# Performance work log

Hardware: AMD Instinct MI355X
Metric: run time of the kernel (lower is better)

The kernel has to match this reference:

```python
import jax, jax.numpy as jnp
import numpy as np

DIM0, DIMO, WIDTH, DEPTH = 64, 16, 128, 6  # depth = number of weight matrices
N = 524288


def setup_inputs() -> dict:
    key = jax.random.key(0)
    ks = jax.random.split(key, DEPTH + 1)
    x = jax.random.normal(ks[0], (N, DIM0), dtype=jnp.float32)
    bd0 = 1.0 / np.sqrt(DIM0)   # first layer init bound (per torch code)
    bd = 1.0 / np.sqrt(WIDTH)   # remaining layers init bound
    W0 = jax.random.uniform(ks[1], (DIM0, WIDTH), minval=-bd0, maxval=bd0, dtype=jnp.float32)
    W1 = jax.random.uniform(ks[2], (WIDTH, WIDTH), minval=-bd, maxval=bd, dtype=jnp.float32)
    W2 = jax.random.uniform(ks[3], (WIDTH, WIDTH), minval=-bd, maxval=bd, dtype=jnp.float32)
    W3 = jax.random.uniform(ks[4], (WIDTH, WIDTH), minval=-bd, maxval=bd, dtype=jnp.float32)
    W4 = jax.random.uniform(ks[5], (WIDTH, WIDTH), minval=-bd, maxval=bd, dtype=jnp.float32)
    W5 = jax.random.uniform(ks[6], (WIDTH, DIMO), minval=-bd, maxval=bd, dtype=jnp.float32)
    bias = jnp.zeros((DIMO,), dtype=jnp.float32)
    return {"x": x, "W0": W0, "W1": W1, "W2": W2, "W3": W3, "W4": W4, "W5": W5, "bias": bias}


def reference(x, W0, W1, W2, W3, W4, W5, bias):
    # Fully-fused MLP math: matmul (no bias) + ReLU for every layer except the
    # last (output_activation='None'); then cast back to x dtype and add bias.
    h = jax.nn.relu(x @ W0)
    h = jax.nn.relu(h @ W1)
    h = jax.nn.relu(h @ W2)
    h = jax.nn.relu(h @ W3)
    h = jax.nn.relu(h @ W4)
    out = (h @ W5).astype(x.dtype) + bias
    return out
```

## Files before the change

### kernel.cpp

```cpp
#include <hip/hip_runtime.h>
#include <stdint.h>


typedef __bf16 bf16x8 __attribute__((ext_vector_type(8)));
typedef __bf16 bf16x4 __attribute__((ext_vector_type(4)));
typedef float  floatx4 __attribute__((ext_vector_type(4)));

constexpr int NS   = 524288;
constexpr int TILE = 128;
constexpr int NBLK = NS / TILE;

constexpr int WTOT = 9472;

__global__ void prep_weights(const float* __restrict__ W0, const float* __restrict__ W1,
                             const float* __restrict__ W2, const float* __restrict__ W3,
                             const float* __restrict__ W4, const float* __restrict__ W5,
                             bf16x8* __restrict__ ws) {
  int gid = blockIdx.x * blockDim.x + threadIdx.x;
  if (gid >= WTOT) return;
  const float* Wsrc; int nout, KT, base;
  if (gid < 1024)      { Wsrc = W0; nout = 128; KT = 2; base = 0;    }
  else if (gid < 3072) { Wsrc = W1; nout = 128; KT = 4; base = 1024; }
  else if (gid < 5120) { Wsrc = W2; nout = 128; KT = 4; base = 3072; }
  else if (gid < 7168) { Wsrc = W3; nout = 128; KT = 4; base = 5120; }
  else if (gid < 9216) { Wsrc = W4; nout = 128; KT = 4; base = 7168; }
  else                 { Wsrc = W5; nout = 16;  KT = 4; base = 9216; }
  int id  = gid - base;
  int p   = id & 63;
  int l15 = p & 15;
  int g   = p >> 4;
  int blk = id >> 6;
  int kt  = blk % KT;
  int it  = blk / KT;
  int row = it * 16 + l15;
  int kc  = kt * 4 + g;
  bf16x8 v;
#pragma unroll
  for (int j = 0; j < 8; ++j)
    v[j] = (__bf16)Wsrc[(8 * kc + j) * nout + row];
  ws[gid] = v;
}

__device__ __forceinline__ void zero_acc(floatx4 acc[4][4]) {
  floatx4 z = {0.f, 0.f, 0.f, 0.f};
#pragma unroll
  for (int i = 0; i < 4; ++i)
#pragma unroll
    for (int j = 0; j < 4; ++j) acc[i][j] = z;
}

template <int KT>
__device__ __forceinline__ void layer_mm(const bf16x8* __restrict__ wg,
                                         const bf16x8* Hb, floatx4 acc[4][4],
                                         int n_base, int l15, int g, int lane) {
#pragma unroll
  for (int kt = 0; kt < KT; ++kt) {
    const int cx = (kt * 4 + g) ^ (l15 & 7);
    bf16x8 a[4], b[4];
#pragma unroll
    for (int i = 0; i < 4; ++i) a[i] = wg[((i * KT + kt) << 6) + lane];
#pragma unroll
    for (int i = 0; i < 4; ++i) b[i] = Hb[(n_base + 16 * i + l15) * 16 + cx];
#pragma unroll
    for (int ot = 0; ot < 4; ++ot)
#pragma unroll
      for (int nt = 0; nt < 4; ++nt)
        acc[ot][nt] = __builtin_amdgcn_mfma_f32_16x16x32_bf16(a[ot], b[nt], acc[ot][nt], 0, 0, 0);
  }
}

__device__ __forceinline__ void write_h(bf16x4* H8, const floatx4 acc[4][4],
                                        int m_base, int n_base, int l15, int g) {
#pragma unroll
  for (int ot = 0; ot < 4; ++ot) {
    int ob    = m_base + 16 * ot + 4 * g;
    int phys8 = (((ob >> 3) ^ (l15 & 7)) << 1) | ((ob >> 2) & 1);
#pragma unroll
    for (int nt = 0; nt < 4; ++nt) {
      int s = n_base + 16 * nt + l15;
      floatx4 v = acc[ot][nt];
      bf16x4 h;
      h[0] = (__bf16)fmaxf(v[0], 0.0f);
      h[1] = (__bf16)fmaxf(v[1], 0.0f);
      h[2] = (__bf16)fmaxf(v[2], 0.0f);
      h[3] = (__bf16)fmaxf(v[3], 0.0f);
      H8[s * 32 + phys8] = h;
    }
  }
}

__global__ void __launch_bounds__(256, 4) mlp_kernel(const float* __restrict__ x,
                                                     const float* __restrict__ bias,
                                                     const bf16x8* __restrict__ wimg,
                                                     float* __restrict__ out) {
  __shared__ bf16x8 Hbuf[TILE * 16];

  const int t    = threadIdx.x;
  const int lane = t & 63;
  const int w    = t >> 6;
  const int l15  = lane & 15;
  const int g    = lane >> 4;
  const int m_half = w & 1;
  const int m_base = m_half * 64;
  const int n_base = (w >> 1) * 64;
  const int tile = blockIdx.x;

  const float* xt = x + (size_t)tile * TILE * 64;
#pragma unroll
  for (int i = 0; i < 4; ++i) {
    int f2 = t + 256 * i;
    int s = f2 >> 3, c = f2 & 7;
    const floatx4* src = (const floatx4*)(xt + f2 * 8);
    floatx4 lo = src[0], hi = src[1];
    bf16x8 v;
    v[0] = (__bf16)lo[0]; v[1] = (__bf16)lo[1]; v[2] = (__bf16)lo[2]; v[3] = (__bf16)lo[3];
    v[4] = (__bf16)hi[0]; v[5] = (__bf16)hi[1]; v[6] = (__bf16)hi[2]; v[7] = (__bf16)hi[3];
    Hbuf[s * 16 + (c ^ (s & 7))] = v;
  }
  __syncthreads();

  floatx4 acc[4][4];

  zero_acc(acc);
  layer_mm<2>(wimg + m_half * 512, Hbuf, acc, n_base, l15, g, lane);
  __syncthreads();
  write_h((bf16x4*)Hbuf, acc, m_base, n_base, l15, g);
  __syncthreads();

  constexpr int WOFF[5] = {1024, 3072, 5120, 7168, 9216};
#pragma unroll
  for (int l = 0; l < 4; ++l) {
    zero_acc(acc);
    layer_mm<4>(wimg + WOFF[l] + m_half * 1024, Hbuf, acc, n_base, l15, g, lane);
    __syncthreads();
    write_h((bf16x4*)Hbuf, acc, m_base, n_base, l15, g);
    __syncthreads();
  }

  floatx4 a5[2];
  {
    floatx4 z = {0.f, 0.f, 0.f, 0.f};
    a5[0] = z; a5[1] = z;
  }
  const int n5 = w * 32;
#pragma unroll
  for (int kt = 0; kt < 4; ++kt) {
    int cx = (kt * 4 + g) ^ (l15 & 7);
    bf16x8 a = wimg[9216 + (kt << 6) + lane];
#pragma unroll
    for (int nt = 0; nt < 2; ++nt) {
      bf16x8 b = Hbuf[(n5 + 16 * nt + l15) * 16 + cx];
      a5[nt] = __builtin_amdgcn_mfma_f32_16x16x32_bf16(a, b, a5[nt], 0, 0, 0);
    }
  }
  floatx4 bv = *(const floatx4*)(bias + 4 * g);
  floatx4* outv = (floatx4*)out;
#pragma unroll
  for (int nt = 0; nt < 2; ++nt) {
    int s = tile * TILE + n5 + 16 * nt + l15;
    outv[s * 4 + g] = a5[nt] + bv;
  }
}

extern "C" void kernel_launch(void* const* d_in, const int* in_sizes, int n_in,
                              void* d_out, int out_size, void* d_ws, size_t ws_size,
                              hipStream_t stream) {
  (void)in_sizes; (void)n_in; (void)out_size; (void)ws_size;
  const float* x    = (const float*)d_in[0];
  const float* W0   = (const float*)d_in[1];
  const float* W1   = (const float*)d_in[2];
  const float* W2   = (const float*)d_in[3];
  const float* W3   = (const float*)d_in[4];
  const float* W4   = (const float*)d_in[5];
  const float* W5   = (const float*)d_in[6];
  const float* bias = (const float*)d_in[7];
  bf16x8* ws = (bf16x8*)d_ws;

  prep_weights<<<(WTOT + 255) / 256, 256, 0, stream>>>(W0, W1, W2, W3, W4, W5, ws);
  mlp_kernel<<<NBLK, 256, 0, stream>>>(x, bias, (const bf16x8*)ws, (float*)d_out);
}
```

Baseline: 282.7 us.

## Give each wave full output width over its own rows and drop block barriers

Repartitions the per-layer GEMM so each wave computes all 128 output features for its own 32 samples, so hidden activations in shared memory are private per wave. This lets all __syncthreads between layers be removed, and the input staging is likewise done per wave. In exchange each wave loads twice as many weight fragments per k-step, and the occupancy hint is lowered from 4 to 3.

```diff
diff --git a/kernel.cpp b/kernel.cpp
--- a/kernel.cpp
+++ b/kernel.cpp
@@ -41,42 +41,42 @@
   ws[gid] = v;
 }
 
-__device__ __forceinline__ void zero_acc(floatx4 acc[4][4]) {
+__device__ __forceinline__ void zero_acc(floatx4 acc[8][2]) {
   floatx4 z = {0.f, 0.f, 0.f, 0.f};
 #pragma unroll
-  for (int i = 0; i < 4; ++i)
-#pragma unroll
-    for (int j = 0; j < 4; ++j) acc[i][j] = z;
+  for (int i = 0; i < 8; ++i) {
+    acc[i][0] = z; acc[i][1] = z;
+  }
 }
 
 template <int KT>
 __device__ __forceinline__ void layer_mm(const bf16x8* __restrict__ wg,
-                                         const bf16x8* Hb, floatx4 acc[4][4],
+                                         const bf16x8* Hb, floatx4 acc[8][2],
                                          int n_base, int l15, int g, int lane) {
 #pragma unroll
   for (int kt = 0; kt < KT; ++kt) {
     const int cx = (kt * 4 + g) ^ (l15 & 7);
-    bf16x8 a[4], b[4];
+    bf16x8 a[8], b[2];
 #pragma unroll
-    for (int i = 0; i < 4; ++i) a[i] = wg[((i * KT + kt) << 6) + lane];
+    for (int i = 0; i < 8; ++i) a[i] = wg[((i * KT + kt) << 6) + lane];
+    b[0] = Hb[(n_base + l15) * 16 + cx];
+    b[1] = Hb[(n_base + 16 + l15) * 16 + cx];
 #pragma unroll
-    for (int i = 0; i < 4; ++i) b[i] = Hb[(n_base + 16 * i + l15) * 16 + cx];
+    for (int ot = 0; ot < 8; ++ot)
 #pragma unroll
-    for (int ot = 0; ot < 4; ++ot)
-#pragma unroll
-      for (int nt = 0; nt < 4; ++nt)
+      for (int nt = 0; nt < 2; ++nt)
         acc[ot][nt] = __builtin_amdgcn_mfma_f32_16x16x32_bf16(a[ot], b[nt], acc[ot][nt], 0, 0, 0);
   }
 }
 
-__device__ __forceinline__ void write_h(bf16x4* H8, const floatx4 acc[4][4],
-                                        int m_base, int n_base, int l15, int g) {
+__device__ __forceinline__ void write_h(bf16x4* H8, const floatx4 acc[8][2],
+                                        int n_base, int l15, int g) {
 #pragma unroll
-  for (int ot = 0; ot < 4; ++ot) {
-    int ob    = m_base + 16 * ot + 4 * g;
+  for (int ot = 0; ot < 8; ++ot) {
+    int ob    = 16 * ot + 4 * g;
     int phys8 = (((ob >> 3) ^ (l15 & 7)) << 1) | ((ob >> 2) & 1);
 #pragma unroll
-    for (int nt = 0; nt < 4; ++nt) {
+    for (int nt = 0; nt < 2; ++nt) {
       int s = n_base + 16 * nt + l15;
       floatx4 v = acc[ot][nt];
       bf16x4 h;
@@ -89,7 +89,7 @@
   }
 }
 
-__global__ void __launch_bounds__(256, 4) mlp_kernel(const float* __restrict__ x,
+__global__ void __launch_bounds__(256, 3) mlp_kernel(const float* __restrict__ x,
                                                      const float* __restrict__ bias,
                                                      const bf16x8* __restrict__ wimg,
                                                      float* __restrict__ out) {
@@ -100,41 +100,34 @@
   const int w    = t >> 6;
   const int l15  = lane & 15;
   const int g    = lane >> 4;
-  const int m_half = w & 1;
-  const int m_base = m_half * 64;
-  const int n_base = (w >> 1) * 64;
+  const int n_base = w * 32;
   const int tile = blockIdx.x;
 
-  const float* xt = x + (size_t)tile * TILE * 64;
+  const float* xt = x + (size_t)tile * TILE * 64 + (size_t)n_base * 64;
 #pragma unroll
   for (int i = 0; i < 4; ++i) {
-    int f2 = t + 256 * i;
+    int f2 = lane + 64 * i;
     int s = f2 >> 3, c = f2 & 7;
     const floatx4* src = (const floatx4*)(xt + f2 * 8);
     floatx4 lo = src[0], hi = src[1];
     bf16x8 v;
     v[0] = (__bf16)lo[0]; v[1] = (__bf16)lo[1]; v[2] = (__bf16)lo[2]; v[3] = (__bf16)lo[3];
     v[4] = (__bf16)hi[0]; v[5] = (__bf16)hi[1]; v[6] = (__bf16)hi[2]; v[7] = (__bf16)hi[3];
-    Hbuf[s * 16 + (c ^ (s & 7))] = v;
+    Hbuf[(n_base + s) * 16 + (c ^ (s & 7))] = v;
   }
-  __syncthreads();
 
-  floatx4 acc[4][4];
+  floatx4 acc[8][2];
 
   zero_acc(acc);
-  layer_mm<2>(wimg + m_half * 512, Hbuf, acc, n_base, l15, g, lane);
-  __syncthreads();
-  write_h((bf16x4*)Hbuf, acc, m_base, n_base, l15, g);
-  __syncthreads();
+  layer_mm<2>(wimg, Hbuf, acc, n_base, l15, g, lane);
+  write_h((bf16x4*)Hbuf, acc, n_base, l15, g);
 
   constexpr int WOFF[5] = {1024, 3072, 5120, 7168, 9216};
 #pragma unroll
   for (int l = 0; l < 4; ++l) {
     zero_acc(acc);
-    layer_mm<4>(wimg + WOFF[l] + m_half * 1024, Hbuf, acc, n_base, l15, g, lane);
-    __syncthreads();
-    write_h((bf16x4*)Hbuf, acc, m_base, n_base, l15, g);
-    __syncthreads();
+    layer_mm<4>(wimg + WOFF[l], Hbuf, acc, n_base, l15, g, lane);
+    write_h((bf16x4*)Hbuf, acc, n_base, l15, g);
   }
 
   floatx4 a5[2];
@@ -142,14 +135,13 @@
     floatx4 z = {0.f, 0.f, 0.f, 0.f};
     a5[0] = z; a5[1] = z;
   }
-  const int n5 = w * 32;
 #pragma unroll
   for (int kt = 0; kt < 4; ++kt) {
     int cx = (kt * 4 + g) ^ (l15 & 7);
     bf16x8 a = wimg[9216 + (kt << 6) + lane];
 #pragma unroll
     for (int nt = 0; nt < 2; ++nt) {
-      bf16x8 b = Hbuf[(n5 + 16 * nt + l15) * 16 + cx];
+      bf16x8 b = Hbuf[(n_base + 16 * nt + l15) * 16 + cx];
       a5[nt] = __builtin_amdgcn_mfma_f32_16x16x32_bf16(a, b, a5[nt], 0, 0, 0);
     }
   }
@@ -157,7 +149,7 @@
   floatx4* outv = (floatx4*)out;
 #pragma unroll
   for (int nt = 0; nt < 2; ++nt) {
-    int s = tile * TILE + n5 + 16 * nt + l15;
+    int s = tile * TILE + n_base + 16 * nt + l15;
     outv[s * 4 + g] = a5[nt] + bv;
   }
 }
```

Result: no change. 280.4 us (-0.8%).
